# Optimization experiments

Hardware: AMD Instinct MI355X
Metric: run time of the kernel (lower is better)

The kernel has to match this reference:

```python
import jax, jax.numpy as jnp
import numpy as np

EPSILON = 1e-8

def setup_inputs() -> dict:
    key = jax.random.key(0)
    k1, k2, k3, k4 = jax.random.split(key, 4)
    B, C_in, C_out, H, W, S, K = 16, 512, 512, 32, 32, 512, 3
    x = jax.random.normal(k1, (B, C_in, H, W), dtype=jnp.float32)
    w = jax.random.normal(k2, (B, S), dtype=jnp.float32)
    # Linear(style_dim -> in_chan), bias initialized to ones per module code
    style_w = jax.random.normal(k3, (C_in, S), dtype=jnp.float32) * (1.0 / np.sqrt(S))
    style_b = jnp.ones((C_in,), dtype=jnp.float32)
    # kaiming_normal_(fan_in, leaky_relu): std = sqrt(2/(1+0.01^2)) / sqrt(fan_in)
    fan_in = C_in * K * K
    gain = np.sqrt(2.0 / (1.0 + 0.01 ** 2))
    weight = jax.random.normal(k4, (C_out, C_in, K, K), dtype=jnp.float32) * (gain / np.sqrt(fan_in))
    return {"x": x, "w": w, "style_w": style_w, "style_b": style_b, "weight": weight}

def reference(x, w, style_w, style_b, weight):
    B, C, H, W_ = x.shape
    C_out, _, K, _ = weight.shape
    # style modulation: Linear(style_dim -> in_chan)
    style = w @ style_w.T + style_b                       # (B, C_in)
    weights = style[:, None, :, None, None] * weight[None]  # (B, C_out, C_in, K, K)
    # demodulation
    d = jax.lax.rsqrt(jnp.sum(weights * weights, axis=(2, 3, 4), keepdims=True) + EPSILON)
    weights = weights * d
    # grouped conv with groups = batch
    pad = 1 if K > 1 else 0
    xg = x.reshape(1, B * C, H, W_)
    wg = weights.reshape(B * C_out, C, K, K)
    y = jax.lax.conv_general_dilated(
        xg, wg, window_strides=(1, 1), padding=((pad, pad), (pad, pad)),
        dimension_numbers=("NCHW", "OIHW", "NCHW"), feature_group_count=B)
    return y.reshape(B, C_out, H, W_)
```

## Files before the change

kernel.cpp:

```cpp
#include <hip/hip_runtime.h>
#include <hip/hip_bf16.h>

#define NB 16
#define CI 512
#define CO 512
#define HW 1024
#define SD 512
#define EPSI 1e-8f

typedef __attribute__((ext_vector_type(8))) short bf16x8;
typedef __attribute__((ext_vector_type(16))) float f32x16;
typedef __attribute__((ext_vector_type(4))) unsigned int u32x4;

#define GLOAD_LDS16(g, l) __builtin_amdgcn_global_load_lds( \
    (const __attribute__((address_space(1))) unsigned int*)(const void*)(g), \
    (__attribute__((address_space(3))) unsigned int*)(void*)(l), 16, 0, 0)
#define SCHED0() __builtin_amdgcn_sched_barrier(0)
#define SBAR()   __builtin_amdgcn_s_barrier()

__global__ void k_prep(const float* __restrict__ w, const float* __restrict__ sw,
                       const float* __restrict__ sb, const float* __restrict__ wt,
                       float* __restrict__ style, float* __restrict__ wsq,
                       __hip_bfloat16* __restrict__ wtb, u32x4* __restrict__ zpage) {
    if (blockIdx.x < 2048) {
        int gw = (blockIdx.x * 256 + threadIdx.x) >> 6;
        int l = threadIdx.x & 63;
        int b = gw >> 9, c = gw & 511;
        const float4* wr = (const float4*)(w + b * SD) + (l << 1);
        const float4* sr = (const float4*)(sw + c * SD) + (l << 1);
        float4 a0 = wr[0], a1 = wr[1], q0 = sr[0], q1 = sr[1];
        float acc = a0.x * q0.x + a0.y * q0.y + a0.z * q0.z + a0.w * q0.w
                  + a1.x * q1.x + a1.y * q1.y + a1.z * q1.z + a1.w * q1.w;
#pragma unroll
        for (int off = 32; off > 0; off >>= 1) acc += __shfl_down(acc, off);
        if (l == 0) style[gw] = acc + sb[c];
    } else {
        if (blockIdx.x == 2048 && threadIdx.x < 64)
            zpage[threadIdx.x] = (u32x4){0, 0, 0, 0};
        int idx = (blockIdx.x - 2048) * 256 + threadIdx.x;
        const float* p = wt + (size_t)idx * 9;
        float a = 0.f;
#pragma unroll
        for (int t = 0; t < 9; ++t) {
            float v = p[t];
            a += v * v;
            wtb[t * (CO * CI) + idx] = __float2bfloat16(v);
        }
        wsq[idx] = a;
    }
}

__global__ void k_demod2(const float* __restrict__ style, const float* __restrict__ wsq,
                         float* __restrict__ dv) {
    int gw = (blockIdx.x * 256 + threadIdx.x) >> 6;
    int l = threadIdx.x & 63;
    int b = gw >> 9, co = gw & 511;
    const float4* st = (const float4*)(style + b * CI) + (l << 1);
    const float4* wq = (const float4*)(wsq + (size_t)co * CI) + (l << 1);
    float4 s0 = st[0], s1 = st[1], q0 = wq[0], q1 = wq[1];
    float acc = s0.x * s0.x * q0.x + s0.y * s0.y * q0.y + s0.z * s0.z * q0.z + s0.w * s0.w * q0.w
              + s1.x * s1.x * q1.x + s1.y * s1.y * q1.y + s1.z * s1.z * q1.z + s1.w * s1.w * q1.w;
#pragma unroll
    for (int off = 32; off > 0; off >>= 1) acc += __shfl_down(acc, off);
    if (l == 0) dv[gw] = rsqrtf(acc + EPSI);
}

__global__ void k_xs(const float* __restrict__ x, const float* __restrict__ style,
                     __hip_bfloat16* __restrict__ xs) {
    __shared__ float tile[32][66];
    int b = blockIdx.z, c0 = blockIdx.y * 64, p0 = blockIdx.x * 32;
    int tx = threadIdx.x & 31, ty = threadIdx.x >> 5;
#pragma unroll
    for (int i = 0; i < 8; ++i) {
        int ci = i * 8 + ty;
        tile[tx][ci] = x[((size_t)b * CI + c0 + ci) * HW + p0 + tx] * style[b * CI + c0 + ci];
    }
    __syncthreads();
    int r = threadIdx.x >> 3, kc = threadIdx.x & 7;
    union { bf16x8 v; __hip_bfloat16 h[8]; } U;
#pragma unroll
    for (int i = 0; i < 8; ++i)
        U.h[i] = __float2bfloat16(tile[r][kc * 8 + i]);
    *(bf16x8*)(xs + ((size_t)b * HW + p0 + r) * CI + c0 + kc * 8) = U.v;
}

#define XS_BYTES 52224
#define WBUF_BYTES 16384
#define SMEM_TOTAL (2 * XS_BYTES + 3 * WBUF_BYTES)

extern "C" __global__ __launch_bounds__(512, 2) void k_conv(
        const __hip_bfloat16* __restrict__ wtb,
        const __hip_bfloat16* __restrict__ xs,
        const float* __restrict__ dvec,
        const char* __restrict__ zpage,
        float* __restrict__ out) {
    extern __shared__ char smem[];
    char* Xs  = smem;
    char* Wsb = smem + 2 * XS_BYTES;

    const int tid  = threadIdx.x;
    const int lane = tid & 63;
    const int wv   = tid >> 6;
    const int wb   = wv >> 2;
    const int wr   = (wv >> 1) & 1;
    const int wn   = wv & 1;

    int bid = blockIdx.x;
    int xcd = bid & 7, idx = bid >> 3;
    int cot = xcd >> 1;
    int px8 = idx & 7;
    int bp  = (idx >> 3) | ((xcd & 1) << 2);
    const int co0 = cot * 128;
    const int p0  = px8 * 128;
    const int y0  = px8 * 4;
    const int b0  = bp * 2;
    const int b   = b0 + wb;

    if (tid < 192) {
        int g = tid & 7;
        int rx = ((tid >> 3) & 1) ? 33 : 0;
        int row = tid >> 4;
        int off = (row * 34 + rx) * 128 + g * 16;
        *(u32x4*)(Xs + off) = (u32x4){0, 0, 0, 0};
        *(u32x4*)(Xs + XS_BYTES + off) = (u32x4){0, 0, 0, 0};
    }

    const int srcgW = (lane & 7) ^ (lane >> 3);

    auto issueW = [&](int tap, int cin, int bufi) {
        const __hip_bfloat16* wsrc = wtb + ((size_t)tap * CO + co0) * CI + cin;
        char* wdst = Wsb + bufi * WBUF_BYTES;
#pragma unroll
        for (int k = 0; k < 2; ++k) {
            int seg = k * 8 + wv;
            int co_l = seg * 8 + (lane >> 3);
            GLOAD_LDS16(wsrc + co_l * CI + srcgW * 8, wdst + seg * 1024);
        }
    };
    auto issueX = [&](char* Xdst, int cin) {
#pragma unroll
        for (int k = 0; k < 6; ++k) {
            int sid = k * 8 + wv;
            int bb = (sid >= 24) ? 1 : 0;
            int rem = sid - bb * 24;
            int ry = rem >> 2, seg = rem & 3;
            int rx0 = 1 + seg * 8;
            char* ldst = Xdst + ((bb * 6 + ry) * 34 + rx0) * 128;
            int y = y0 - 1 + ry;
            int rx = rx0 + (lane >> 3);
            int srcg = (lane & 7) ^ (rx & 7);
            if ((unsigned)y < 32u)
                GLOAD_LDS16(xs + ((size_t)(b0 + bb) * HW + (y << 5) + (rx - 1)) * CI + cin + srcg * 8, ldst);
            else
                GLOAD_LDS16(zpage, ldst);
        }
    };

    f32x16 acc[2][2];
#pragma unroll
    for (int m = 0; m < 2; ++m)
#pragma unroll
        for (int n = 0; n < 2; ++n)
            acc[m][n] = (f32x16)(0.f);

    issueW(0, 0, 0);
    issueW(1, 0, 1);
    issueX(Xs, 0);
    SCHED0();
    asm volatile("s_waitcnt lgkmcnt(0) vmcnt(0)" ::: "memory");
    SCHED0();
    SBAR();
    SCHED0();

    for (int cc = 0; cc < 8; ++cc) {
        const char* Xcur = Xs + (cc & 1) * XS_BYTES;
#pragma unroll
        for (int t = 0; t < 9; ++t) {
            if (!(cc == 7 && t >= 7)) {
                const int tn  = (t <= 6) ? (t + 2) : (t - 7);
                const int cin = ((t <= 6) ? cc : (cc + 1)) * 64;
                issueW(tn, cin, (t + 2) % 3);
            }
            if (t == 0 && cc < 7)
                issueX(Xs + ((cc + 1) & 1) * XS_BYTES, (cc + 1) * 64);
            SCHED0();

            const char* Wb = Wsb + (t % 3) * WBUF_BYTES;
            const int ky = t / 3, kx = t - (t / 3) * 3;
            __builtin_amdgcn_s_setprio(1);
#pragma unroll
            for (int q = 0; q < 4; ++q) {
                bf16x8 afr[2], bfr[2];
                int g = (q << 1) + (lane >> 5);
#pragma unroll
                for (int m = 0; m < 2; ++m) {
                    int cr = wr * 64 + m * 32 + (lane & 31);
                    afr[m] = *(const bf16x8*)(Wb + cr * 128 + ((g ^ (cr & 7)) << 4));
                }
#pragma unroll
                for (int n = 0; n < 2; ++n) {
                    int ry = wn * 2 + n + ky;
                    int rx = (lane & 31) + kx;
                    bfr[n] = *(const bf16x8*)(Xcur + ((wb * 6 + ry) * 34 + rx) * 128 +
                                              ((g ^ (rx & 7)) << 4));
                }
#pragma unroll
                for (int m = 0; m < 2; ++m)
#pragma unroll
                    for (int n = 0; n < 2; ++n)
                        acc[m][n] = __builtin_amdgcn_mfma_f32_32x32x16_bf16(afr[m], bfr[n], acc[m][n], 0, 0, 0);
            }
            __builtin_amdgcn_s_setprio(0);

            if (!(cc == 7 && t == 8)) {
                SCHED0();
                if (cc < 7 && t < 2)
                    asm volatile("s_waitcnt lgkmcnt(0) vmcnt(8)" ::: "memory");
                else if (cc == 7 && t == 7)
                    asm volatile("s_waitcnt lgkmcnt(0) vmcnt(0)" ::: "memory");
                else
                    asm volatile("s_waitcnt lgkmcnt(0) vmcnt(2)" ::: "memory");
                SCHED0();
                SBAR();
                SCHED0();
            }
        }
    }

#pragma unroll
    for (int m = 0; m < 2; ++m) {
#pragma unroll
        for (int r = 0; r < 16; ++r) {
            int co = co0 + wr * 64 + m * 32 + (r & 3) + ((r >> 2) << 3) + ((lane >> 5) << 2);
            float dvv = dvec[b * CO + co];
            float* orow = out + ((size_t)b * CO + co) * HW + p0 + wn * 64;
            orow[lane & 31]        = acc[m][0][r] * dvv;
            orow[32 + (lane & 31)] = acc[m][1][r] * dvv;
        }
    }
}

extern "C" void kernel_launch(void* const* d_in, const int* in_sizes, int n_in,
                              void* d_out, int out_size, void* d_ws, size_t ws_size,
                              hipStream_t stream) {
    const float* x  = (const float*)d_in[0];
    const float* w  = (const float*)d_in[1];
    const float* sw = (const float*)d_in[2];
    const float* sb = (const float*)d_in[3];
    const float* wt = (const float*)d_in[4];
    float* out = (float*)d_out;

    char* ws = (char*)d_ws;
    float* style = (float*)(ws);
    float* dvec  = (float*)(ws + 32768);
    float* wsq   = (float*)(ws + 65536);
    __hip_bfloat16* wtb = (__hip_bfloat16*)(ws + 1114112);
    __hip_bfloat16* xsb = (__hip_bfloat16*)(ws + 5832704);
    char* zpage = ws + 22609920;

    hipFuncSetAttribute((const void*)k_conv,
                        hipFuncAttributeMaxDynamicSharedMemorySize, SMEM_TOTAL);

    k_prep<<<3072, 256, 0, stream>>>(w, sw, sb, wt, style, wsq,
                                     (__hip_bfloat16*)wtb, (u32x4*)zpage);
    k_xs<<<dim3(32, 8, 16), 256, 0, stream>>>(x, style, xsb);
    k_demod2<<<2048, 256, 0, stream>>>(style, wsq, dvec);
    k_conv<<<256, 512, SMEM_TOTAL, stream>>>(wtb, xsb, dvec, zpage, out);
}
```

Before: 91.39 us.

## Split K across wave halves with LDS reduction, widen per-wave tile to 128x64

Each block now handles one batch and a 256-pixel tile (8 rows) instead of two batches at 128 pixels. Each wave computes the full 128 output channels over 64 pixels, using half of each 64-channel K slice. The two wave halves combine their partial accumulators through LDS at the end. The goal is fewer A-fragment reloads per MFMA and a smaller X staging buffer, at the cost of twice as many accumulator registers and an extra LDS reduction pass.

Result: no change. 90.00 us (-1.5%).

```diff
diff --git a/kernel.cpp b/kernel.cpp
--- a/kernel.cpp
+++ b/kernel.cpp
@@ -84,7 +84,7 @@
     *(bf16x8*)(xs + ((size_t)b * HW + p0 + r) * CI + c0 + kc * 8) = U.v;
 }
 
-#define XS_BYTES 52224
+#define XS_BYTES 43520
 #define WBUF_BYTES 16384
 #define SMEM_TOTAL (2 * XS_BYTES + 3 * WBUF_BYTES)
 
@@ -100,29 +100,26 @@
 
     const int tid  = threadIdx.x;
     const int lane = tid & 63;
+    const int l31  = lane & 31;
     const int wv   = tid >> 6;
-    const int wb   = wv >> 2;
-    const int wr   = (wv >> 1) & 1;
-    const int wn   = wv & 1;
+    const int kh   = wv >> 2;
+    const int wn   = wv & 3;
 
     int bid = blockIdx.x;
     int xcd = bid & 7, idx = bid >> 3;
-    int cot = xcd >> 1;
-    int px8 = idx & 7;
-    int bp  = (idx >> 3) | ((xcd & 1) << 2);
+    const int cot = xcd >> 1;
+    const int px4 = idx & 3;
+    const int b   = (idx >> 2) | ((xcd & 1) << 3);
     const int co0 = cot * 128;
-    const int p0  = px8 * 128;
-    const int y0  = px8 * 4;
-    const int b0  = bp * 2;
-    const int b   = b0 + wb;
-
-    if (tid < 192) {
-        int g = tid & 7;
-        int rx = ((tid >> 3) & 1) ? 33 : 0;
-        int row = tid >> 4;
-        int off = (row * 34 + rx) * 128 + g * 16;
-        *(u32x4*)(Xs + off) = (u32x4){0, 0, 0, 0};
-        *(u32x4*)(Xs + XS_BYTES + off) = (u32x4){0, 0, 0, 0};
+    const int p0  = px4 * 256;
+    const int y0  = px4 * 8;
+
+    if (tid < 320) {
+        int bufi = tid / 160, r = tid % 160;
+        int g = r & 7;
+        int rx = (r & 8) ? 33 : 0;
+        int row = r >> 4;
+        *(u32x4*)(Xs + bufi * XS_BYTES + (row * 34 + rx) * 128 + g * 16) = (u32x4){0, 0, 0, 0};
     }
 
     const int srcgW = (lane & 7) ^ (lane >> 3);
@@ -139,26 +136,24 @@
     };
     auto issueX = [&](char* Xdst, int cin) {
 #pragma unroll
-        for (int k = 0; k < 6; ++k) {
-            int sid = k * 8 + wv;
-            int bb = (sid >= 24) ? 1 : 0;
-            int rem = sid - bb * 24;
-            int ry = rem >> 2, seg = rem & 3;
-            int rx0 = 1 + seg * 8;
-            char* ldst = Xdst + ((bb * 6 + ry) * 34 + rx0) * 128;
+        for (int k = 0; k < 5; ++k) {
+            int u = k * 8 + wv;
+            int ry = u >> 2, sub = u & 3;
+            int rx0 = 1 + sub * 8;
+            char* ldst = Xdst + (ry * 34 + rx0) * 128;
             int y = y0 - 1 + ry;
             int rx = rx0 + (lane >> 3);
             int srcg = (lane & 7) ^ (rx & 7);
             if ((unsigned)y < 32u)
-                GLOAD_LDS16(xs + ((size_t)(b0 + bb) * HW + (y << 5) + (rx - 1)) * CI + cin + srcg * 8, ldst);
+                GLOAD_LDS16(xs + ((size_t)b * HW + (y << 5) + (rx - 1)) * CI + cin + srcg * 8, ldst);
             else
                 GLOAD_LDS16(zpage, ldst);
         }
     };
 
-    f32x16 acc[2][2];
-#pragma unroll
-    for (int m = 0; m < 2; ++m)
+    f32x16 acc[4][2];
+#pragma unroll
+    for (int m = 0; m < 4; ++m)
 #pragma unroll
         for (int n = 0; n < 2; ++n)
             acc[m][n] = (f32x16)(0.f);
@@ -189,53 +184,84 @@
             const int ky = t / 3, kx = t - (t / 3) * 3;
             __builtin_amdgcn_s_setprio(1);
 #pragma unroll
-            for (int q = 0; q < 4; ++q) {
-                bf16x8 afr[2], bfr[2];
-                int g = (q << 1) + (lane >> 5);
-#pragma unroll
-                for (int m = 0; m < 2; ++m) {
-                    int cr = wr * 64 + m * 32 + (lane & 31);
+            for (int ql = 0; ql < 2; ++ql) {
+                int g = kh * 4 + ql * 2 + (lane >> 5);
+                bf16x8 afr[4], bfr[2];
+#pragma unroll
+                for (int m = 0; m < 4; ++m) {
+                    int cr = m * 32 + l31;
                     afr[m] = *(const bf16x8*)(Wb + cr * 128 + ((g ^ (cr & 7)) << 4));
                 }
 #pragma unroll
                 for (int n = 0; n < 2; ++n) {
-                    int ry = wn * 2 + n + ky;
-                    int rx = (lane & 31) + kx;
-                    bfr[n] = *(const bf16x8*)(Xcur + ((wb * 6 + ry) * 34 + rx) * 128 +
-                                              ((g ^ (rx & 7)) << 4));
-                }
-#pragma unroll
-                for (int m = 0; m < 2; ++m)
+                    int row = wn * 2 + n + ky;
+                    int rx = l31 + kx;
+                    bfr[n] = *(const bf16x8*)(Xcur + (row * 34 + rx) * 128 + ((g ^ (rx & 7)) << 4));
+                }
+#pragma unroll
+                for (int m = 0; m < 4; ++m)
 #pragma unroll
                     for (int n = 0; n < 2; ++n)
                         acc[m][n] = __builtin_amdgcn_mfma_f32_32x32x16_bf16(afr[m], bfr[n], acc[m][n], 0, 0, 0);
             }
             __builtin_amdgcn_s_setprio(0);
 
-            if (!(cc == 7 && t == 8)) {
-                SCHED0();
-                if (cc < 7 && t < 2)
-                    asm volatile("s_waitcnt lgkmcnt(0) vmcnt(8)" ::: "memory");
-                else if (cc == 7 && t == 7)
-                    asm volatile("s_waitcnt lgkmcnt(0) vmcnt(0)" ::: "memory");
-                else
-                    asm volatile("s_waitcnt lgkmcnt(0) vmcnt(2)" ::: "memory");
-                SCHED0();
-                SBAR();
-                SCHED0();
-            }
-        }
-    }
-
-#pragma unroll
-    for (int m = 0; m < 2; ++m) {
-#pragma unroll
-        for (int r = 0; r < 16; ++r) {
-            int co = co0 + wr * 64 + m * 32 + (r & 3) + ((r >> 2) << 3) + ((lane >> 5) << 2);
-            float dvv = dvec[b * CO + co];
-            float* orow = out + ((size_t)b * CO + co) * HW + p0 + wn * 64;
-            orow[lane & 31]        = acc[m][0][r] * dvv;
-            orow[32 + (lane & 31)] = acc[m][1][r] * dvv;
+            SCHED0();
+            if (cc == 7 && t == 8) {
+                asm volatile("s_waitcnt lgkmcnt(0)" ::: "memory");
+            } else if (cc < 7 && t < 2) {
+                asm volatile("s_waitcnt lgkmcnt(0) vmcnt(7)" ::: "memory");
+            } else if (cc == 7 && t == 7) {
+                asm volatile("s_waitcnt lgkmcnt(0) vmcnt(0)" ::: "memory");
+            } else {
+                asm volatile("s_waitcnt lgkmcnt(0) vmcnt(2)" ::: "memory");
+            }
+            SCHED0();
+            SBAR();
+            SCHED0();
+        }
+    }
+
+    if (kh) {
+        char* rb = smem + wn * 32768;
+#pragma unroll
+        for (int m = 0; m < 4; ++m)
+#pragma unroll
+            for (int n = 0; n < 2; ++n)
+#pragma unroll
+                for (int g4 = 0; g4 < 4; ++g4) {
+                    float4 v = make_float4(acc[m][n][g4 * 4 + 0], acc[m][n][g4 * 4 + 1],
+                                           acc[m][n][g4 * 4 + 2], acc[m][n][g4 * 4 + 3]);
+                    *(float4*)(rb + ((((m * 2 + n) * 4 + g4) * 64) + lane) * 16) = v;
+                }
+    }
+    SCHED0();
+    asm volatile("s_waitcnt lgkmcnt(0)" ::: "memory");
+    SCHED0();
+    SBAR();
+    SCHED0();
+    if (!kh) {
+        char* rb = smem + wn * 32768;
+#pragma unroll
+        for (int m = 0; m < 4; ++m) {
+#pragma unroll
+            for (int n = 0; n < 2; ++n)
+#pragma unroll
+                for (int g4 = 0; g4 < 4; ++g4) {
+                    float4 v = *(const float4*)(rb + ((((m * 2 + n) * 4 + g4) * 64) + lane) * 16);
+                    acc[m][n][g4 * 4 + 0] += v.x;
+                    acc[m][n][g4 * 4 + 1] += v.y;
+                    acc[m][n][g4 * 4 + 2] += v.z;
+                    acc[m][n][g4 * 4 + 3] += v.w;
+                }
+#pragma unroll
+            for (int r = 0; r < 16; ++r) {
+                int col = m * 32 + (r & 3) + ((r >> 2) << 3) + ((lane >> 5) << 2);
+                float dvv = dvec[b * CO + co0 + col];
+                float* orow = out + ((size_t)b * CO + co0 + col) * HW + p0 + wn * 64;
+                orow[l31]      = acc[m][0][r] * dvv;
+                orow[32 + l31] = acc[m][1][r] * dvv;
+            }
         }
     }
 }
```

## Prefetch LDS fragments into registers one tap ahead and merge xs/demod kernels

Applied to the files above, without the earlier changes.

The conv main loop now loads the next tap's A/B fragments from LDS into registers right after the barrier, then runs the MFMAs on the previously loaded fragments. This overlaps LDS reads with matrix math, and the X and W global-to-LDS prefetch schedule is reworked to match (one more tap of lookahead, X issued two chunks ahead). Separately, the k_xs and k_demod2 kernels are merged into one launch to save a kernel launch. The cost is a doubled fragment register set (32 bf16x8 values), which at 512 threads and 2 blocks per CU may raise register pressure, and the reworked buffer indexing carries a risk of data races.

Result: slower. 97.84 us (+7.1%).

```diff
diff --git a/kernel.cpp b/kernel.cpp
--- a/kernel.cpp
+++ b/kernel.cpp
@@ -50,38 +50,38 @@
     }
 }
 
-__global__ void k_demod2(const float* __restrict__ style, const float* __restrict__ wsq,
-                         float* __restrict__ dv) {
-    int gw = (blockIdx.x * 256 + threadIdx.x) >> 6;
-    int l = threadIdx.x & 63;
-    int b = gw >> 9, co = gw & 511;
-    const float4* st = (const float4*)(style + b * CI) + (l << 1);
-    const float4* wq = (const float4*)(wsq + (size_t)co * CI) + (l << 1);
-    float4 s0 = st[0], s1 = st[1], q0 = wq[0], q1 = wq[1];
-    float acc = s0.x * s0.x * q0.x + s0.y * s0.y * q0.y + s0.z * s0.z * q0.z + s0.w * s0.w * q0.w
-              + s1.x * s1.x * q1.x + s1.y * s1.y * q1.y + s1.z * s1.z * q1.z + s1.w * s1.w * q1.w;
-#pragma unroll
-    for (int off = 32; off > 0; off >>= 1) acc += __shfl_down(acc, off);
-    if (l == 0) dv[gw] = rsqrtf(acc + EPSI);
-}
-
-__global__ void k_xs(const float* __restrict__ x, const float* __restrict__ style,
-                     __hip_bfloat16* __restrict__ xs) {
+__global__ void k_xs2(const float* __restrict__ x, const float* __restrict__ style,
+                      const float* __restrict__ wsq, __hip_bfloat16* __restrict__ xs,
+                      float* __restrict__ dv) {
     __shared__ float tile[32][66];
-    int b = blockIdx.z, c0 = blockIdx.y * 64, p0 = blockIdx.x * 32;
-    int tx = threadIdx.x & 31, ty = threadIdx.x >> 5;
-#pragma unroll
-    for (int i = 0; i < 8; ++i) {
-        int ci = i * 8 + ty;
-        tile[tx][ci] = x[((size_t)b * CI + c0 + ci) * HW + p0 + tx] * style[b * CI + c0 + ci];
-    }
-    __syncthreads();
-    int r = threadIdx.x >> 3, kc = threadIdx.x & 7;
-    union { bf16x8 v; __hip_bfloat16 h[8]; } U;
-#pragma unroll
-    for (int i = 0; i < 8; ++i)
-        U.h[i] = __float2bfloat16(tile[r][kc * 8 + i]);
-    *(bf16x8*)(xs + ((size_t)b * HW + p0 + r) * CI + c0 + kc * 8) = U.v;
+    if (blockIdx.x < 4096) {
+        int b = blockIdx.x >> 8, c0 = ((blockIdx.x >> 5) & 7) * 64, p0 = (blockIdx.x & 31) * 32;
+        int tx = threadIdx.x & 31, ty = threadIdx.x >> 5;
+#pragma unroll
+        for (int i = 0; i < 8; ++i) {
+            int ci = i * 8 + ty;
+            tile[tx][ci] = x[((size_t)b * CI + c0 + ci) * HW + p0 + tx] * style[b * CI + c0 + ci];
+        }
+        __syncthreads();
+        int r = threadIdx.x >> 3, kc = threadIdx.x & 7;
+        union { bf16x8 v; __hip_bfloat16 h[8]; } U;
+#pragma unroll
+        for (int i = 0; i < 8; ++i)
+            U.h[i] = __float2bfloat16(tile[r][kc * 8 + i]);
+        *(bf16x8*)(xs + ((size_t)b * HW + p0 + r) * CI + c0 + kc * 8) = U.v;
+    } else {
+        int gw = ((blockIdx.x - 4096) * 256 + threadIdx.x) >> 6;
+        int l = threadIdx.x & 63;
+        int b = gw >> 9, co = gw & 511;
+        const float4* st = (const float4*)(style + b * CI) + (l << 1);
+        const float4* wq = (const float4*)(wsq + (size_t)co * CI) + (l << 1);
+        float4 s0 = st[0], s1 = st[1], q0 = wq[0], q1 = wq[1];
+        float acc = s0.x * s0.x * q0.x + s0.y * s0.y * q0.y + s0.z * s0.z * q0.z + s0.w * s0.w * q0.w
+                  + s1.x * s1.x * q1.x + s1.y * s1.y * q1.y + s1.z * s1.z * q1.z + s1.w * s1.w * q1.w;
+#pragma unroll
+        for (int off = 32; off > 0; off >>= 1) acc += __shfl_down(acc, off);
+        if (l == 0) dv[gw] = rsqrtf(acc + EPSI);
+    }
 }
 
 #define XS_BYTES 52224
@@ -100,6 +100,7 @@
 
     const int tid  = threadIdx.x;
     const int lane = tid & 63;
+    const int l31  = lane & 31;
     const int wv   = tid >> 6;
     const int wb   = wv >> 2;
     const int wr   = (wv >> 1) & 1;
@@ -163,6 +164,69 @@
         for (int n = 0; n < 2; ++n)
             acc[m][n] = (f32x16)(0.f);
 
+    bf16x8 fa[4][2], fb[4][2];
+
+#define LOADFRAGS(T2, XB)                                                         \
+    {                                                                             \
+        const char* Wb_ = Wsb + ((T2) % 3) * WBUF_BYTES;                          \
+        _Pragma("unroll")                                                         \
+        for (int q = 0; q < 4; ++q) {                                             \
+            int g = (q << 1) + (lane >> 5);                                       \
+            _Pragma("unroll")                                                     \
+            for (int m = 0; m < 2; ++m) {                                         \
+                int cr = wr * 64 + m * 32 + l31;                                  \
+                fa[q][m] = *(const bf16x8*)(Wb_ + cr * 128 + ((g ^ (cr & 7)) << 4)); \
+            }                                                                     \
+            _Pragma("unroll")                                                     \
+            for (int n = 0; n < 2; ++n) {                                         \
+                int ry = wn * 2 + n + ((T2) / 3);                                 \
+                int rx = l31 + ((T2) % 3);                                        \
+                fb[q][n] = *(const bf16x8*)((XB) + ((wb * 6 + ry) * 34 + rx) * 128 + \
+                                            ((g ^ (rx & 7)) << 4));               \
+            }                                                                     \
+        }                                                                         \
+    }
+
+#define DOMFMA()                                                                  \
+    {                                                                             \
+        __builtin_amdgcn_s_setprio(1);                                            \
+        _Pragma("unroll")                                                         \
+        for (int q = 0; q < 4; ++q)                                               \
+            _Pragma("unroll")                                                     \
+            for (int m = 0; m < 2; ++m)                                           \
+                _Pragma("unroll")                                                 \
+                for (int n = 0; n < 2; ++n)                                       \
+                    acc[m][n] = __builtin_amdgcn_mfma_f32_32x32x16_bf16(          \
+                        fa[q][m], fb[q][n], acc[m][n], 0, 0, 0);                  \
+        __builtin_amdgcn_s_setprio(0);                                            \
+    }
+
+#define STAGE(T)                                                                  \
+    {                                                                             \
+        SBAR(); SCHED0();                                                         \
+        asm volatile("s_waitcnt lgkmcnt(0)" ::: "memory"); SCHED0();              \
+        DOMFMA();                                                                 \
+        if (!((T) == 8 && cc == 7)) {                                             \
+            SCHED0();                                                             \
+            if ((T) == 0) {                                                       \
+                if (cc < 7) asm volatile("s_waitcnt vmcnt(8)" ::: "memory");      \
+                else        asm volatile("s_waitcnt vmcnt(2)" ::: "memory");      \
+            } else if ((T) == 7) {                                                \
+                if (cc == 7) asm volatile("s_waitcnt vmcnt(0)" ::: "memory");     \
+                else         asm volatile("s_waitcnt vmcnt(2)" ::: "memory");     \
+            } else {                                                              \
+                asm volatile("s_waitcnt vmcnt(2)" ::: "memory");                  \
+            }                                                                     \
+            SCHED0(); SBAR(); SCHED0();                                           \
+            if ((T) < 8) { LOADFRAGS((T) + 1, Xcur); }                            \
+            else         { LOADFRAGS(0, Xnxt); }                                  \
+            if ((T) == 8 && cc <= 5) issueX(Xcur, (cc + 2) * 64);                 \
+            if (cc < 7 || (T) <= 5)                                               \
+                issueW(((T) + 3) % 9, (((T) >= 6) ? cc + 1 : cc) * 64, (T) % 3);  \
+            SCHED0();                                                             \
+        }                                                                         \
+    }
+
     issueW(0, 0, 0);
     issueW(1, 0, 1);
     issueX(Xs, 0);
@@ -171,60 +235,16 @@
     SCHED0();
     SBAR();
     SCHED0();
+    LOADFRAGS(0, Xs);
+    issueX(Xs + XS_BYTES, 64);
+    issueW(2, 0, 2);
+    SCHED0();
 
     for (int cc = 0; cc < 8; ++cc) {
-        const char* Xcur = Xs + (cc & 1) * XS_BYTES;
-#pragma unroll
-        for (int t = 0; t < 9; ++t) {
-            if (!(cc == 7 && t >= 7)) {
-                const int tn  = (t <= 6) ? (t + 2) : (t - 7);
-                const int cin = ((t <= 6) ? cc : (cc + 1)) * 64;
-                issueW(tn, cin, (t + 2) % 3);
-            }
-            if (t == 0 && cc < 7)
-                issueX(Xs + ((cc + 1) & 1) * XS_BYTES, (cc + 1) * 64);
-            SCHED0();
-
-            const char* Wb = Wsb + (t % 3) * WBUF_BYTES;
-            const int ky = t / 3, kx = t - (t / 3) * 3;
-            __builtin_amdgcn_s_setprio(1);
-#pragma unroll
-            for (int q = 0; q < 4; ++q) {
-                bf16x8 afr[2], bfr[2];
-                int g = (q << 1) + (lane >> 5);
-#pragma unroll
-                for (int m = 0; m < 2; ++m) {
-                    int cr = wr * 64 + m * 32 + (lane & 31);
-                    afr[m] = *(const bf16x8*)(Wb + cr * 128 + ((g ^ (cr & 7)) << 4));
-                }
-#pragma unroll
-                for (int n = 0; n < 2; ++n) {
-                    int ry = wn * 2 + n + ky;
-                    int rx = (lane & 31) + kx;
-                    bfr[n] = *(const bf16x8*)(Xcur + ((wb * 6 + ry) * 34 + rx) * 128 +
-                                              ((g ^ (rx & 7)) << 4));
-                }
-#pragma unroll
-                for (int m = 0; m < 2; ++m)
-#pragma unroll
-                    for (int n = 0; n < 2; ++n)
-                        acc[m][n] = __builtin_amdgcn_mfma_f32_32x32x16_bf16(afr[m], bfr[n], acc[m][n], 0, 0, 0);
-            }
-            __builtin_amdgcn_s_setprio(0);
-
-            if (!(cc == 7 && t == 8)) {
-                SCHED0();
-                if (cc < 7 && t < 2)
-                    asm volatile("s_waitcnt lgkmcnt(0) vmcnt(8)" ::: "memory");
-                else if (cc == 7 && t == 7)
-                    asm volatile("s_waitcnt lgkmcnt(0) vmcnt(0)" ::: "memory");
-                else
-                    asm volatile("s_waitcnt lgkmcnt(0) vmcnt(2)" ::: "memory");
-                SCHED0();
-                SBAR();
-                SCHED0();
-            }
-        }
+        char* Xcur = Xs + (cc & 1) * XS_BYTES;
+        char* Xnxt = Xs + ((cc + 1) & 1) * XS_BYTES;
+        STAGE(0) STAGE(1) STAGE(2) STAGE(3) STAGE(4)
+        STAGE(5) STAGE(6) STAGE(7) STAGE(8)
     }
 
 #pragma unroll
@@ -263,7 +283,6 @@
 
     k_prep<<<3072, 256, 0, stream>>>(w, sw, sb, wt, style, wsq,
                                      (__hip_bfloat16*)wtb, (u32x4*)zpage);
-    k_xs<<<dim3(32, 8, 16), 256, 0, stream>>>(x, style, xsb);
-    k_demod2<<<2048, 256, 0, stream>>>(style, wsq, dvec);
+    k_xs2<<<6144, 256, 0, stream>>>(x, style, wsq, xsb, dvec);
     k_conv<<<256, 512, SMEM_TOTAL, stream>>>(wtb, xsb, dvec, zpage, out);
 }
```
